# Optimization experiments

Measured on AMD Instinct MI355X. Metric: run time of the kernel, lower is better.

Reference implementation:

```python
import jax, jax.numpy as jnp
import numpy as np


def setup_inputs() -> dict:
    key = jax.random.key(0)
    k1, k2, k3 = jax.random.split(key, 3)
    T, B, H = 2048, 16, 512
    inputs = jax.random.normal(k1, (T, B, H), dtype=jnp.float32)
    # torch.rand override of the context vector, made explicit/deterministic
    rand_ctx = jax.random.uniform(k2, (T, B, H), dtype=jnp.float32)
    # xavier_uniform_ with relu gain: bound = gain * sqrt(6/(fan_in+fan_out))
    gain = float(np.sqrt(2.0))
    bound = gain * float(np.sqrt(6.0 / (H + H)))
    W = jax.random.uniform(k3, (H, H), dtype=jnp.float32, minval=-bound, maxval=bound)
    return {"inputs": inputs, "rand_ctx": rand_ctx, "W": W, "attention_width": 3}


def reference(inputs, rand_ctx, W, attention_width):
    # inputs: [T, B, H]; attention_width is dead code in the original (lb=0 always)
    T, B, H = inputs.shape
    # Context half of the output: inputs[t] for t<2, random override for t>=2
    t_col = jnp.arange(T)[:, None, None]
    ctx = jnp.where(t_col < 2, inputs, rand_ctx)               # [T, B, H]
    results = jnp.concatenate([inputs, ctx], axis=-1)          # [T, B, 2H]

    # Attention weights (detached in the original, never fed to the output):
    # scores[b, t, s] = (x_t W) . x_s, softmax over s < t, only for t >= 2
    q = jnp.einsum('tbh,hk->tbk', inputs, W)                   # [T, B, H]
    scores = jnp.einsum('tbk,sbk->bts', q, inputs)             # [B, T, T]
    t_idx = jnp.arange(T)
    mask = (t_idx[None, :] < t_idx[:, None]) & (t_idx[:, None] >= 2)  # [T, T]
    neg = jnp.finfo(scores.dtype).min
    attn = jax.nn.softmax(jnp.where(mask[None], scores, neg), axis=-1)
    attn = jnp.where(mask[None], attn, jnp.zeros((), scores.dtype))   # zero padded rows
    return results, attn
```

## Files before the change

kernel.cpp:

```cpp
#include <hip/hip_runtime.h>
#include <math.h>

#define T_DIM 2048
#define B_DIM 16
#define H_DIM 512
#define NKB   (H_DIM / 32)

typedef _Float16 f16x8 __attribute__((ext_vector_type(8)));
typedef float f32x4 __attribute__((ext_vector_type(4)));

__device__ __forceinline__ unsigned short h_bits(_Float16 h) {
    unsigned short u; __builtin_memcpy(&u, &h, 2); return u;
}

__device__ __forceinline__ size_t tile_off(int rowblk, int kblk) {
    return ((size_t)rowblk * NKB + kblk) * 4096;
}
__device__ __forceinline__ size_t tiled_idx(int r, int c) {
    return tile_off(r >> 7, c >> 5) + (size_t)((c >> 3) & 3) * 1024 + (size_t)(r & 127) * 8 + (c & 7);
}

__global__ __launch_bounds__(256) void k_prep(const float* __restrict__ X,
                                              const float* __restrict__ RC,
                                              float* __restrict__ out,
                                              unsigned short* __restrict__ Xh) {
    int i = blockIdx.x * 256 + threadIdx.x;
    int row = i >> 6;
    int h0 = (i & 63) * 8;
    int t = row >> 4;
    int b = row & 15;
    const float* xp = X + (size_t)row * H_DIM + h0;
    float4 v0 = *(const float4*)xp;
    float4 v1 = *(const float4*)(xp + 4);
    float* op = out + (size_t)row * (2 * H_DIM) + h0;
    *(float4*)op = v0;
    *(float4*)(op + 4) = v1;
    const float* cp = RC + (size_t)row * H_DIM + h0;
    float4 c0 = *(const float4*)cp;
    float4 c1 = *(const float4*)(cp + 4);
    if (t < 2) { c0 = v0; c1 = v1; }
    *(float4*)(op + H_DIM) = c0;
    *(float4*)(op + H_DIM + 4) = c1;
    float xs[8] = {v0.x, v0.y, v0.z, v0.w, v1.x, v1.y, v1.z, v1.w};
    unsigned int hw[4];
#pragma unroll
    for (int e = 0; e < 4; ++e) {
        _Float16 a = (_Float16)xs[2 * e], bb = (_Float16)xs[2 * e + 1];
        hw[e] = (unsigned int)h_bits(a) | ((unsigned int)h_bits(bb) << 16);
    }
    int r = b * T_DIM + t;
    *(uint4*)(Xh + tiled_idx(r, h0)) = make_uint4(hw[0], hw[1], hw[2], hw[3]);
}

__global__ __launch_bounds__(256) void k_split_w(const float* __restrict__ W,
                                                 unsigned short* __restrict__ Wth) {
    int i = blockIdx.x * 256 + threadIdx.x;
    int n = i & 511;
    int k0 = (i >> 9) * 8;
    unsigned int hw[4];
#pragma unroll
    for (int e = 0; e < 4; ++e) {
        _Float16 h0 = (_Float16)W[(size_t)(k0 + 2 * e) * H_DIM + n];
        _Float16 h1 = (_Float16)W[(size_t)(k0 + 2 * e + 1) * H_DIM + n];
        hw[e] = (unsigned int)h_bits(h0) | ((unsigned int)h_bits(h1) << 16);
    }
    *(uint4*)(Wth + tiled_idx(n, k0)) = make_uint4(hw[0], hw[1], hw[2], hw[3]);
}

__device__ __forceinline__ void stage_half(const unsigned short* __restrict__ src_tile,
                                           unsigned short* lds_base, int lane, int h) {
#pragma unroll
    for (int c = 0; c < 4; ++c) {
        const int ch = h * 4 + c;
        __builtin_amdgcn_global_load_lds(
            (const __attribute__((address_space(1))) void*)(src_tile + ch * 512 + lane * 8),
            (__attribute__((address_space(3))) void*)(lds_base + ch * 512),
            16, 0, 0);
    }
}

__global__ __launch_bounds__(256) void k_qgemm_mfma(const unsigned short* __restrict__ Xh,
                                                    const unsigned short* __restrict__ Wth,
                                                    unsigned short* __restrict__ Qh) {
    __shared__ __align__(16) unsigned short Ah[2][4][128][8], Bh[2][4][128][8];
    const int bid = blockIdx.x;
    const int swz = (bid & 7) * 128 + (bid >> 3);
    const int mblk = swz >> 2, nblk = swz & 3;
    const int m0 = mblk * 128, n0 = nblk * 128;
    const int tid = threadIdx.x, lane = tid & 63, w = tid >> 6;
    const int t_off = (w >> 1) * 64, s_off = (w & 1) * 64;
    const int l15 = lane & 15, lg = lane >> 4;
    f32x4 acc[4][4] = {};

    for (int ksp = 0; ksp < NKB / 2; ++ksp) {
        if (ksp) __syncthreads();
        if (w < 2) {
            stage_half(Xh + tile_off(mblk, 2 * ksp),     &Ah[0][0][0][0], lane, w);
            stage_half(Xh + tile_off(mblk, 2 * ksp + 1), &Ah[1][0][0][0], lane, w);
        } else {
            stage_half(Wth + tile_off(nblk, 2 * ksp),     &Bh[0][0][0][0], lane, w - 2);
            stage_half(Wth + tile_off(nblk, 2 * ksp + 1), &Bh[1][0][0][0], lane, w - 2);
        }
        __syncthreads();

#pragma unroll
        for (int kk = 0; kk < 2; ++kk) {
            f16x8 ah[4], bh[4];
#pragma unroll
            for (int i2 = 0; i2 < 4; ++i2)
                ah[i2] = *(const f16x8*)&Ah[kk][lg][t_off + i2 * 16 + l15][0];
#pragma unroll
            for (int j = 0; j < 4; ++j)
                bh[j] = *(const f16x8*)&Bh[kk][lg][s_off + j * 16 + l15][0];
#pragma unroll
            for (int i2 = 0; i2 < 4; ++i2)
#pragma unroll
                for (int j = 0; j < 4; ++j)
                    acc[i2][j] = __builtin_amdgcn_mfma_f32_16x16x32_f16(ah[i2], bh[j], acc[i2][j], 0, 0, 0);
        }
    }

#pragma unroll
    for (int i2 = 0; i2 < 4; ++i2)
#pragma unroll
        for (int j = 0; j < 4; ++j)
#pragma unroll
            for (int r = 0; r < 4; ++r) {
                int R = m0 + t_off + i2 * 16 + lg * 4 + r;
                int C = n0 + s_off + j * 16 + l15;
                _Float16 qh = (_Float16)acc[i2][j][r];
                Qh[tiled_idx(R, C)] = h_bits(qh);
            }
}

__global__ __launch_bounds__(256) void k_scores_mfma(const unsigned short* __restrict__ Qh,
                                                     const unsigned short* __restrict__ Xh,
                                                     float* __restrict__ attn) {
    const int bid = blockIdx.x;
    const int swz = (bid & 7) * 272 + (bid >> 3);
    const int b = swz / 136;
    const int r = swz - b * 136;
    int ti = (int)((sqrtf(8.f * (float)r + 1.f) - 1.f) * 0.5f);
    while ((ti + 1) * (ti + 2) / 2 <= r) ++ti;
    while (ti * (ti + 1) / 2 > r) --ti;
    const int si = r - ti * (ti + 1) / 2;
    const int t0 = ti * 128, s0 = si * 128;

    __shared__ __align__(16) unsigned short Ah[2][4][128][8], Bh[2][4][128][8];
    const int tid = threadIdx.x, lane = tid & 63, w = tid >> 6;
    const int t_off = (w >> 1) * 64, s_off = (w & 1) * 64;
    const int l15 = lane & 15, lg = lane >> 4;
    const int ablk = b * (T_DIM / 128) + ti;
    const int bblk = b * (T_DIM / 128) + si;
    f32x4 acc[4][4] = {};

    for (int ksp = 0; ksp < NKB / 2; ++ksp) {
        if (ksp) __syncthreads();
        if (w < 2) {
            stage_half(Qh + tile_off(ablk, 2 * ksp),     &Ah[0][0][0][0], lane, w);
            stage_half(Qh + tile_off(ablk, 2 * ksp + 1), &Ah[1][0][0][0], lane, w);
        } else {
            stage_half(Xh + tile_off(bblk, 2 * ksp),     &Bh[0][0][0][0], lane, w - 2);
            stage_half(Xh + tile_off(bblk, 2 * ksp + 1), &Bh[1][0][0][0], lane, w - 2);
        }
        __syncthreads();

#pragma unroll
        for (int kk = 0; kk < 2; ++kk) {
            f16x8 ah[4], bh[4];
#pragma unroll
            for (int i2 = 0; i2 < 4; ++i2)
                ah[i2] = *(const f16x8*)&Ah[kk][lg][t_off + i2 * 16 + l15][0];
#pragma unroll
            for (int j = 0; j < 4; ++j)
                bh[j] = *(const f16x8*)&Bh[kk][lg][s_off + j * 16 + l15][0];
#pragma unroll
            for (int i2 = 0; i2 < 4; ++i2)
#pragma unroll
                for (int j = 0; j < 4; ++j)
                    acc[i2][j] = __builtin_amdgcn_mfma_f32_16x16x32_f16(ah[i2], bh[j], acc[i2][j], 0, 0, 0);
        }
    }

    float* base = attn + (size_t)b * T_DIM * T_DIM;
#pragma unroll
    for (int i2 = 0; i2 < 4; ++i2)
#pragma unroll
        for (int j = 0; j < 4; ++j)
#pragma unroll
            for (int rr = 0; rr < 4; ++rr) {
                int t = t0 + t_off + i2 * 16 + lg * 4 + rr;
                int s = s0 + s_off + j * 16 + l15;
                base[(size_t)t * T_DIM + s] = acc[i2][j][rr];
            }
}

__global__ __launch_bounds__(256) void k_softmax(float* __restrict__ attn) {
    const int row = blockIdx.x;
    const int t = row & (T_DIM - 1);
    float* p = attn + (size_t)row * T_DIM;
    const int tid = threadIdx.x;
    const int n = (t >= 2) ? t : 0;
    __shared__ float redm[4], redl[4];

    if (n == 0) {
        const float4 z = {0.f, 0.f, 0.f, 0.f};
        for (int s = tid * 4; s < T_DIM; s += 1024) *(float4*)&p[s] = z;
        return;
    }

    float m = -1e30f, l = 0.f;
    for (int s = tid * 4; s < n; s += 1024) {
        float v[4];
        int cnt;
        if (s + 3 < n) {
            float4 q = *(const float4*)&p[s];
            v[0] = q.x; v[1] = q.y; v[2] = q.z; v[3] = q.w; cnt = 4;
        } else {
            cnt = n - s;
            for (int j = 0; j < cnt; ++j) v[j] = p[s + j];
        }
        float vm = v[0];
        for (int j = 1; j < cnt; ++j) vm = fmaxf(vm, v[j]);
        if (vm > m) { l *= expf(m - vm); m = vm; }
        for (int j = 0; j < cnt; ++j) l += expf(v[j] - m);
    }
#pragma unroll
    for (int off = 32; off >= 1; off >>= 1) {
        float mo = __shfl_xor(m, off);
        float lo = __shfl_xor(l, off);
        float M = fmaxf(m, mo);
        l = l * expf(m - M) + lo * expf(mo - M);
        m = M;
    }
    if ((tid & 63) == 0) { redm[tid >> 6] = m; redl[tid >> 6] = l; }
    __syncthreads();
    {
        float M = fmaxf(fmaxf(redm[0], redm[1]), fmaxf(redm[2], redm[3]));
        float L = redl[0] * expf(redm[0] - M) + redl[1] * expf(redm[1] - M)
                + redl[2] * expf(redm[2] - M) + redl[3] * expf(redm[3] - M);
        m = M;
        l = L;
    }
    const float inv = 1.f / l;

    for (int s = tid * 4; s < T_DIM; s += 1024) {
        float4 o = {0.f, 0.f, 0.f, 0.f};
        if (s + 3 < n) {
            float4 v = *(float4*)&p[s];
            o.x = expf(v.x - m) * inv;
            o.y = expf(v.y - m) * inv;
            o.z = expf(v.z - m) * inv;
            o.w = expf(v.w - m) * inv;
        } else if (s < n) {
            float tmp[4] = {0.f, 0.f, 0.f, 0.f};
            for (int j = 0; j < 4; ++j)
                if (s + j < n) tmp[j] = expf(p[s + j] - m) * inv;
            o.x = tmp[0]; o.y = tmp[1]; o.z = tmp[2]; o.w = tmp[3];
        }
        *(float4*)&p[s] = o;
    }
}

extern "C" void kernel_launch(void* const* d_in, const int* in_sizes, int n_in,
                              void* d_out, int out_size, void* d_ws, size_t ws_size,
                              hipStream_t stream) {
    const float* inputs   = (const float*)d_in[0];
    const float* rand_ctx = (const float*)d_in[1];
    const float* W        = (const float*)d_in[2];
    float* out  = (float*)d_out;
    float* attn = out + (size_t)T_DIM * B_DIM * 2 * H_DIM;

    unsigned short* Xh  = (unsigned short*)d_ws;
    unsigned short* Qh  = Xh + (size_t)33554432;
    unsigned short* Wth = Xh + (size_t)67108864;

    k_prep<<<dim3(T_DIM * B_DIM * 64 / 256), dim3(256), 0, stream>>>(
        inputs, rand_ctx, out, Xh);

    k_split_w<<<dim3(128), dim3(256), 0, stream>>>(W, Wth);

    k_qgemm_mfma<<<dim3(1024), dim3(256), 0, stream>>>(Xh, Wth, Qh);

    k_scores_mfma<<<dim3(2176), dim3(256), 0, stream>>>(Qh, Xh, attn);

    k_softmax<<<dim3(B_DIM * T_DIM), dim3(256), 0, stream>>>(attn);
}
```

Before: 302.2 us.

## Fuse per-tile softmax max/sum into scores epilogue, drop softmax stats pass

The scores GEMM epilogue now computes, for each row of its 128x128 tile, the masked row max and exp-sum using shuffles and shared memory. It writes these partials to a small workspace buffer indexed by (batch, row, key tile). The softmax kernel then merges up to 16 partials with one wavefront reduction instead of re-reading the whole row to find max and sum. This removes one full read pass over the large fp32 attention matrix, at the cost of extra exp work and a barrier in the scores epilogue.

After: 311.9 us. +3.2%, slower.

```diff
diff --git a/kernel.cpp b/kernel.cpp
--- a/kernel.cpp
+++ b/kernel.cpp
@@ -135,7 +135,8 @@
 
 __global__ __launch_bounds__(256) void k_scores_mfma(const unsigned short* __restrict__ Qh,
                                                      const unsigned short* __restrict__ Xh,
-                                                     float* __restrict__ attn) {
+                                                     float* __restrict__ attn,
+                                                     float2* __restrict__ PML) {
     const int bid = blockIdx.x;
     const int swz = (bid & 7) * 272 + (bid >> 3);
     const int b = swz / 136;
@@ -147,6 +148,7 @@
     const int t0 = ti * 128, s0 = si * 128;
 
     __shared__ __align__(16) unsigned short Ah[2][4][128][8], Bh[2][4][128][8];
+    __shared__ float sm_m[4][64], sm_l[4][64];
     const int tid = threadIdx.x, lane = tid & 63, w = tid >> 6;
     const int t_off = (w >> 1) * 64, s_off = (w & 1) * 64;
     const int l15 = lane & 15, lg = lane >> 4;
@@ -186,22 +188,54 @@
 #pragma unroll
     for (int i2 = 0; i2 < 4; ++i2)
 #pragma unroll
-        for (int j = 0; j < 4; ++j)
-#pragma unroll
-            for (int rr = 0; rr < 4; ++rr) {
-                int t = t0 + t_off + i2 * 16 + lg * 4 + rr;
-                int s = s0 + s_off + j * 16 + l15;
-                base[(size_t)t * T_DIM + s] = acc[i2][j][rr];
+        for (int rr = 0; rr < 4; ++rr) {
+            const int t = t0 + t_off + i2 * 16 + lg * 4 + rr;
+            float vj[4];
+            bool ok[4];
+            float mloc = -1e30f;
+#pragma unroll
+            for (int j = 0; j < 4; ++j) {
+                const int s = s0 + s_off + j * 16 + l15;
+                vj[j] = acc[i2][j][rr];
+                ok[j] = (s < t) && (t >= 2);
+                base[(size_t)t * T_DIM + s] = vj[j];
+                if (ok[j]) mloc = fmaxf(mloc, vj[j]);
             }
-}
-
-__global__ __launch_bounds__(256) void k_softmax(float* __restrict__ attn) {
+#pragma unroll
+            for (int off = 1; off <= 8; off <<= 1)
+                mloc = fmaxf(mloc, __shfl_xor(mloc, off));
+            float lloc = 0.f;
+#pragma unroll
+            for (int j = 0; j < 4; ++j)
+                if (ok[j]) lloc += expf(vj[j] - mloc);
+#pragma unroll
+            for (int off = 1; off <= 8; off <<= 1)
+                lloc += __shfl_xor(lloc, off);
+            if (l15 == 0) {
+                const int lr = i2 * 16 + lg * 4 + rr;
+                sm_m[w][lr] = mloc;
+                sm_l[w][lr] = lloc;
+            }
+        }
+    __syncthreads();
+    if (tid < 128) {
+        const int w0 = (tid >> 6) * 2;
+        const int lr = tid & 63;
+        float m1 = sm_m[w0][lr], l1 = sm_l[w0][lr];
+        float m2 = sm_m[w0 + 1][lr], l2 = sm_l[w0 + 1][lr];
+        float M = fmaxf(m1, m2);
+        float L = l1 * expf(m1 - M) + l2 * expf(m2 - M);
+        PML[(size_t)(b * T_DIM + t0 + tid) * 16 + si] = make_float2(M, L);
+    }
+}
+
+__global__ __launch_bounds__(256) void k_softmax(float* __restrict__ attn,
+                                                 const float2* __restrict__ PML) {
     const int row = blockIdx.x;
     const int t = row & (T_DIM - 1);
     float* p = attn + (size_t)row * T_DIM;
     const int tid = threadIdx.x;
     const int n = (t >= 2) ? t : 0;
-    __shared__ float redm[4], redl[4];
 
     if (n == 0) {
         const float4 z = {0.f, 0.f, 0.f, 0.f};
@@ -209,38 +243,20 @@
         return;
     }
 
+    const int ti = t >> 7;
+    const int ln = tid & 63;
     float m = -1e30f, l = 0.f;
-    for (int s = tid * 4; s < n; s += 1024) {
-        float v[4];
-        int cnt;
-        if (s + 3 < n) {
-            float4 q = *(const float4*)&p[s];
-            v[0] = q.x; v[1] = q.y; v[2] = q.z; v[3] = q.w; cnt = 4;
-        } else {
-            cnt = n - s;
-            for (int j = 0; j < cnt; ++j) v[j] = p[s + j];
-        }
-        float vm = v[0];
-        for (int j = 1; j < cnt; ++j) vm = fmaxf(vm, v[j]);
-        if (vm > m) { l *= expf(m - vm); m = vm; }
-        for (int j = 0; j < cnt; ++j) l += expf(v[j] - m);
-    }
-#pragma unroll
-    for (int off = 32; off >= 1; off >>= 1) {
+    if (ln <= ti) {
+        float2 pm = PML[(size_t)row * 16 + ln];
+        m = pm.x; l = pm.y;
+    }
+#pragma unroll
+    for (int off = 1; off <= 32; off <<= 1) {
         float mo = __shfl_xor(m, off);
         float lo = __shfl_xor(l, off);
         float M = fmaxf(m, mo);
         l = l * expf(m - M) + lo * expf(mo - M);
         m = M;
-    }
-    if ((tid & 63) == 0) { redm[tid >> 6] = m; redl[tid >> 6] = l; }
-    __syncthreads();
-    {
-        float M = fmaxf(fmaxf(redm[0], redm[1]), fmaxf(redm[2], redm[3]));
-        float L = redl[0] * expf(redm[0] - M) + redl[1] * expf(redm[1] - M)
-                + redl[2] * expf(redm[2] - M) + redl[3] * expf(redm[3] - M);
-        m = M;
-        l = L;
     }
     const float inv = 1.f / l;
 
@@ -272,6 +288,7 @@
     float* attn = out + (size_t)T_DIM * B_DIM * 2 * H_DIM;
 
     unsigned short* Xh  = (unsigned short*)d_ws;
+    float2*         PML = (float2*)(Xh + (size_t)16777216);
     unsigned short* Qh  = Xh + (size_t)33554432;
     unsigned short* Wth = Xh + (size_t)67108864;
 
@@ -282,7 +299,7 @@
 
     k_qgemm_mfma<<<dim3(1024), dim3(256), 0, stream>>>(Xh, Wth, Qh);
 
-    k_scores_mfma<<<dim3(2176), dim3(256), 0, stream>>>(Qh, Xh, attn);
-
-    k_softmax<<<dim3(B_DIM * T_DIM), dim3(256), 0, stream>>>(attn);
-}
+    k_scores_mfma<<<dim3(2176), dim3(256), 0, stream>>>(Qh, Xh, attn, PML);
+
+    k_softmax<<<dim3(B_DIM * T_DIM), dim3(256), 0, stream>>>(attn, PML);
+}
```
